# Performance work log

Measured on AMD Instinct MI355X. Metric: run time of the kernel, lower is better.

## Reference

```python
import jax, jax.numpy as jnp
import numpy as np

N, E, IN_DIM, H, C, ED = 100000, 1600000, 128, 8, 16, 16
LN_EPS = 1e-5


def setup_inputs() -> dict:
    key = jax.random.key(0)
    ks = jax.random.split(key, 12)
    s_in = 1.0 / np.sqrt(IN_DIM)
    s_ed = 1.0 / np.sqrt(ED)
    return {
        "edge_index": jax.random.randint(ks[0], (2, E), 0, N, dtype=jnp.int64),
        "point_attr": jax.random.normal(ks[1], (N, IN_DIM), dtype=jnp.float32),
        "edge_attr": jax.random.normal(ks[2], (E, ED), dtype=jnp.float32),
        "W": jax.random.normal(ks[3], (IN_DIM, H * C), dtype=jnp.float32) * s_in,
        "att_src": jax.random.normal(ks[4], (1, H, C), dtype=jnp.float32) * 0.1,
        "att_dst": jax.random.normal(ks[5], (1, H, C), dtype=jnp.float32) * 0.1,
        "W_edge": jax.random.normal(ks[6], (ED, H * C), dtype=jnp.float32) * s_ed,
        "att_edge": jax.random.normal(ks[7], (1, H, C), dtype=jnp.float32) * 0.1,
        "bias": jnp.zeros((H * C,), dtype=jnp.float32),
        "ln_node_g": jnp.ones((H * C,), dtype=jnp.float32),
        "ln_node_b": jnp.zeros((H * C,), dtype=jnp.float32),
        "ln_edge_g": jnp.ones((H,), dtype=jnp.float32),
        "ln_edge_b": jnp.zeros((H,), dtype=jnp.float32),
        "edge_w": jax.random.normal(ks[8], (H, 1), dtype=jnp.float32) / np.sqrt(H),
        "edge_b": jnp.zeros((1,), dtype=jnp.float32),
    }


def _layer_norm(x, g, b):
    mu = jnp.mean(x, axis=-1, keepdims=True)
    var = jnp.mean((x - mu) ** 2, axis=-1, keepdims=True)
    return (x - mu) * jax.lax.rsqrt(var + LN_EPS) * g + b


def reference(edge_index, point_attr, edge_attr, W, att_src, att_dst, W_edge,
              att_edge, bias, ln_node_g, ln_node_b, ln_edge_g, ln_edge_b,
              edge_w, edge_b):
    src, dst = edge_index[0], edge_index[1]
    x = (point_attr @ W).reshape(N, H, C)                 # [N,H,C]
    a_src = jnp.sum(x * att_src, axis=-1)                 # [N,H]
    a_dst = jnp.sum(x * att_dst, axis=-1)                 # [N,H]
    e = (edge_attr @ W_edge).reshape(E, H, C)             # [E,H,C]
    a_edge = jnp.sum(e * att_edge, axis=-1)               # [E,H]
    alpha = jax.nn.leaky_relu(a_src[src] + a_dst[dst] + a_edge, 0.2)
    # segment softmax over destination neighborhoods
    m = jax.ops.segment_max(alpha, dst, num_segments=N)
    m = jnp.where(jnp.isfinite(m), m, 0.0)
    ex = jnp.exp(alpha - m[dst])
    den = jax.ops.segment_sum(ex, dst, num_segments=N)
    alpha_n = ex / (den[dst] + 1e-16)                     # [E,H]
    msg = x[src] * alpha_n[..., None]                     # [E,H,C]
    out = jax.ops.segment_sum(msg, dst, num_segments=N).reshape(N, H * C) + bias
    node_out = jax.nn.leaky_relu(_layer_norm(out, ln_node_g, ln_node_b), 0.01)
    edge_h = _layer_norm(alpha_n, ln_edge_g, ln_edge_b)
    edge_out = jax.nn.relu(edge_h @ edge_w + edge_b)[:, 0]  # [E]
    return node_out, edge_out
```

## Files before the change

kernel.cpp:

```cpp
#include <hip/hip_runtime.h>
#include <hip/hip_bf16.h>

#define NN 100000
#define EE 1600000
#define LN_EPS 1e-5f

__device__ __forceinline__ float bf_lo(unsigned u) {
  union { unsigned i; float f; } c; c.i = u << 16; return c.f;
}
__device__ __forceinline__ float bf_hi(unsigned u) {
  union { unsigned i; float f; } c; c.i = u & 0xffff0000u; return c.f;
}
__device__ __forceinline__ float us_bf(unsigned short u) {
  union { unsigned i; float f; } c; c.i = ((unsigned)u) << 16; return c.f;
}
__device__ __forceinline__ unsigned short f2bf(float f) {
  union { float f; unsigned i; } c; c.f = f;
  unsigned b = c.i + 0x7fffu + ((c.i >> 16) & 1u);
  return (unsigned short)(b >> 16);
}
__device__ __forceinline__ float lrelu02(float v) { return v >= 0.f ? v : 0.2f * v; }

__global__ void k_detect(const void* __restrict__ ei, int* __restrict__ flag) {
  if (threadIdx.x == 0 && blockIdx.x == 0) {
    const unsigned long long* p = (const unsigned long long*)ei;
    int ok = 1;
    for (int i = 0; i < 256; ++i)
      if (p[i] >= (unsigned long long)NN) { ok = 0; break; }
    *flag = ok;
  }
}

__global__ __launch_bounds__(256) void k_convert_hist(const void* __restrict__ ei,
                                                      const int* __restrict__ flag,
                                                      int* __restrict__ idx32,
                                                      int* __restrict__ counts,
                                                      int* __restrict__ rank) {
  int gid = blockIdx.x * 256 + threadIdx.x;
  if (gid >= EE) return;
  int s, d;
  if (*flag) {
    s = (int)((const long long*)ei)[gid];
    d = (int)((const long long*)ei)[EE + gid];
  } else {
    s = ((const int*)ei)[gid];
    d = ((const int*)ei)[EE + gid];
  }
  idx32[gid] = s;
  idx32[EE + gid] = d;
  rank[gid] = atomicAdd(&counts[(unsigned)d * 16], 1);
}

__global__ __launch_bounds__(512) void k_gemm_node(
    const float* __restrict__ P, const float* __restrict__ W,
    const float* __restrict__ attS, const float* __restrict__ attD,
    unsigned* __restrict__ xb, unsigned short* __restrict__ a_srcb,
    unsigned short* __restrict__ a_dstb, int nrows) {
  __shared__ float Rl[32 * 66];
  int t = threadIdx.x;
  int w = __builtin_amdgcn_readfirstlane(t >> 6);
  int l = t & 63;
  int rb = blockIdx.x * 64;
  int cb = w * 16;
  float acc[16];
#pragma unroll
  for (int j = 0; j < 16; ++j) acc[j] = 0.f;

  for (int kc = 0; kc < 4; ++kc) {
    __syncthreads();
    {
      int row = t >> 3;
      int k0 = (t & 7) * 4;
      int grow = rb + row;
      float4 v = make_float4(0.f, 0.f, 0.f, 0.f);
      if (grow < nrows)
        v = *(const float4*)(P + (size_t)grow * 128 + kc * 32 + k0);
      Rl[(k0 + 0) * 66 + row] = v.x;
      Rl[(k0 + 1) * 66 + row] = v.y;
      Rl[(k0 + 2) * 66 + row] = v.z;
      Rl[(k0 + 3) * 66 + row] = v.w;
    }
    __syncthreads();
    const float* Wp = W + (size_t)(kc * 32) * 128 + cb;
#pragma unroll 8
    for (int k = 0; k < 32; ++k) {
      float rv = Rl[k * 66 + l];
#pragma unroll
      for (int j = 0; j < 16; ++j) acc[j] = fmaf(rv, Wp[k * 128 + j], acc[j]);
    }
  }
  int row = rb + l;
  if (row < nrows) {
    float sa = 0.f, sd = 0.f;
#pragma unroll
    for (int j = 0; j < 16; ++j) {
      sa = fmaf(acc[j], attS[cb + j], sa);
      sd = fmaf(acc[j], attD[cb + j], sd);
    }
    a_srcb[(size_t)row * 8 + w] = f2bf(sa);
    a_dstb[(size_t)row * 8 + w] = f2bf(sd);
    unsigned pk[8];
#pragma unroll
    for (int m = 0; m < 8; ++m)
      pk[m] = (unsigned)f2bf(acc[2 * m]) | ((unsigned)f2bf(acc[2 * m + 1]) << 16);
    unsigned* xo = xb + (size_t)row * 64 + cb / 2;
    *(uint4*)(xo) = make_uint4(pk[0], pk[1], pk[2], pk[3]);
    *(uint4*)(xo + 4) = make_uint4(pk[4], pk[5], pk[6], pk[7]);
  }
}

__global__ __launch_bounds__(256) void k_blocksum(const int* __restrict__ counts,
                                                  int* __restrict__ partials, int n) {
  __shared__ int sm[256];
  int t = threadIdx.x;
  int gid = blockIdx.x * 256 + t;
  sm[t] = gid < n ? counts[(unsigned)gid * 16] : 0;
  __syncthreads();
  for (int s = 128; s > 0; s >>= 1) {
    if (t < s) sm[t] += sm[t + s];
    __syncthreads();
  }
  if (t == 0) partials[blockIdx.x] = sm[0];
}

__global__ __launch_bounds__(512) void k_scanpartials(int* __restrict__ partials, int nb) {
  __shared__ int sm[512];
  int t = threadIdx.x;
  int v = t < nb ? partials[t] : 0;
  sm[t] = v;
  __syncthreads();
  for (int off = 1; off < 512; off <<= 1) {
    int u = (t >= off) ? sm[t - off] : 0;
    __syncthreads();
    sm[t] += u;
    __syncthreads();
  }
  if (t < nb) partials[t] = sm[t] - v;
}

__global__ __launch_bounds__(256) void k_scanfinal(const int* __restrict__ counts,
                                                   const int* __restrict__ partials,
                                                   int* __restrict__ offsets, int n) {
  __shared__ int sm[256];
  int t = threadIdx.x;
  int gid = blockIdx.x * 256 + t;
  int v = gid < n ? counts[(unsigned)gid * 16] : 0;
  sm[t] = v;
  __syncthreads();
  for (int off = 1; off < 256; off <<= 1) {
    int u = (t >= off) ? sm[t - off] : 0;
    __syncthreads();
    sm[t] += u;
    __syncthreads();
  }
  int excl = partials[blockIdx.x] + sm[t] - v;
  if (gid < n) offsets[gid] = excl;
  if (gid == n - 1) offsets[n] = excl + v;
}

__global__ __launch_bounds__(256) void k_edgeprep(
    const float* __restrict__ EA, const float* __restrict__ Wedge,
    const float* __restrict__ attE, const int* __restrict__ src,
    const int* __restrict__ dst, const unsigned short* __restrict__ a_srcb,
    const int* __restrict__ offsets, const int* __restrict__ rank,
    unsigned* __restrict__ rec) {
  __shared__ float M[16][8];
  int t = threadIdx.x;
  if (t < 128) {
    int d = t >> 3, h = t & 7;
    float s = 0.f;
#pragma unroll
    for (int c = 0; c < 16; ++c)
      s = fmaf(Wedge[d * 128 + h * 16 + c], attE[h * 16 + c], s);
    M[d][h] = s;
  }
  __syncthreads();
  int stride = gridDim.x * 256;
  for (int e = blockIdx.x * 256 + t; e < EE; e += stride) {
    int sv = src[e], dv = dst[e];
    int rk = rank[e];
    int off = offsets[dv];
    uint4 as4 = *(const uint4*)(a_srcb + (unsigned)sv * 8);
    float ea[16];
    const float4* ea4 = (const float4*)(EA + (size_t)e * 16);
#pragma unroll
    for (int i = 0; i < 4; ++i) {
      float4 v = ea4[i];
      ea[i * 4] = v.x; ea[i * 4 + 1] = v.y; ea[i * 4 + 2] = v.z; ea[i * 4 + 3] = v.w;
    }
    unsigned asu[4] = {as4.x, as4.y, as4.z, as4.w};
    unsigned pk[4];
#pragma unroll
    for (int m = 0; m < 4; ++m) {
      float s0 = 0.f, s1 = 0.f;
#pragma unroll
      for (int d = 0; d < 16; ++d) {
        s0 = fmaf(ea[d], M[d][2 * m], s0);
        s1 = fmaf(ea[d], M[d][2 * m + 1], s1);
      }
      s0 += bf_lo(asu[m]);
      s1 += bf_hi(asu[m]);
      pk[m] = (unsigned)f2bf(s0) | ((unsigned)f2bf(s1) << 16);
    }
    unsigned pos = (unsigned)(off + rk);
    unsigned* rp = rec + (size_t)pos * 8;
    *(uint4*)(rp) = make_uint4(pk[0], pk[1], pk[2], pk[3]);
    *(uint4*)(rp + 4) = make_uint4((unsigned)sv, (unsigned)e, (unsigned)dv, 0u);
  }
}

__global__ __launch_bounds__(512) void k_megaagg(
    const int* __restrict__ offsets, const unsigned* __restrict__ rec,
    const unsigned short* __restrict__ a_dstb, const unsigned* __restrict__ xb,
    const float* __restrict__ bias, const float* __restrict__ g,
    const float* __restrict__ b, const float* __restrict__ eg,
    const float* __restrict__ ebv_, const float* __restrict__ ew,
    const float* __restrict__ ebias, float* __restrict__ node_out,
    float* __restrict__ edge_out) {
  int w = threadIdx.x >> 6, l = threadIdx.x & 63;
  int n = blockIdx.x * 8 + w;
  if (n >= NN) return;
  int s = offsets[n], e = offsets[n + 1];
  int qt = l >> 4, ql = l & 15;
  int h = ql >> 1;
  int hsel = (ql >> 1) & 1;
  unsigned hw = (unsigned)(ql >> 2);
  float ad = us_bf(a_dstb[(unsigned)n * 8 + h]);
  float dn0 = 0.f, dn1 = 0.f, dn2 = 0.f, dn3 = 0.f;
  float acc[8] = {0.f, 0.f, 0.f, 0.f, 0.f, 0.f, 0.f, 0.f};
  int i = s + qt;
  for (; i + 12 < e; i += 16) {
    const unsigned* rA = rec + (unsigned)i * 8u;
    const unsigned* rB = rec + (unsigned)(i + 4) * 8u;
    const unsigned* rC = rec + (unsigned)(i + 8) * 8u;
    const unsigned* rD = rec + (unsigned)(i + 12) * 8u;
    unsigned auA = rA[hw]; unsigned svA = rA[4];
    unsigned auB = rB[hw]; unsigned svB = rB[4];
    unsigned auC = rC[hw]; unsigned svC = rC[4];
    unsigned auD = rD[hw]; unsigned svD = rD[4];
    uint4 xA = *(const uint4*)(xb + svA * 64u + (unsigned)(ql * 4));
    uint4 xB = *(const uint4*)(xb + svB * 64u + (unsigned)(ql * 4));
    uint4 xC = *(const uint4*)(xb + svC * 64u + (unsigned)(ql * 4));
    uint4 xD = *(const uint4*)(xb + svD * 64u + (unsigned)(ql * 4));
    float aA = hsel ? bf_hi(auA) : bf_lo(auA);
    float aB = hsel ? bf_hi(auB) : bf_lo(auB);
    float aC = hsel ? bf_hi(auC) : bf_lo(auC);
    float aD = hsel ? bf_hi(auD) : bf_lo(auD);
    float eA = __expf(lrelu02(aA + ad));
    float eB = __expf(lrelu02(aB + ad));
    float eC = __expf(lrelu02(aC + ad));
    float eD = __expf(lrelu02(aD + ad));
    dn0 += eA; dn1 += eB; dn2 += eC; dn3 += eD;
    acc[0] = fmaf(eA, bf_lo(xA.x), acc[0]); acc[1] = fmaf(eA, bf_hi(xA.x), acc[1]);
    acc[2] = fmaf(eA, bf_lo(xA.y), acc[2]); acc[3] = fmaf(eA, bf_hi(xA.y), acc[3]);
    acc[4] = fmaf(eA, bf_lo(xA.z), acc[4]); acc[5] = fmaf(eA, bf_hi(xA.z), acc[5]);
    acc[6] = fmaf(eA, bf_lo(xA.w), acc[6]); acc[7] = fmaf(eA, bf_hi(xA.w), acc[7]);
    acc[0] = fmaf(eB, bf_lo(xB.x), acc[0]); acc[1] = fmaf(eB, bf_hi(xB.x), acc[1]);
    acc[2] = fmaf(eB, bf_lo(xB.y), acc[2]); acc[3] = fmaf(eB, bf_hi(xB.y), acc[3]);
    acc[4] = fmaf(eB, bf_lo(xB.z), acc[4]); acc[5] = fmaf(eB, bf_hi(xB.z), acc[5]);
    acc[6] = fmaf(eB, bf_lo(xB.w), acc[6]); acc[7] = fmaf(eB, bf_hi(xB.w), acc[7]);
    acc[0] = fmaf(eC, bf_lo(xC.x), acc[0]); acc[1] = fmaf(eC, bf_hi(xC.x), acc[1]);
    acc[2] = fmaf(eC, bf_lo(xC.y), acc[2]); acc[3] = fmaf(eC, bf_hi(xC.y), acc[3]);
    acc[4] = fmaf(eC, bf_lo(xC.z), acc[4]); acc[5] = fmaf(eC, bf_hi(xC.z), acc[5]);
    acc[6] = fmaf(eC, bf_lo(xC.w), acc[6]); acc[7] = fmaf(eC, bf_hi(xC.w), acc[7]);
    acc[0] = fmaf(eD, bf_lo(xD.x), acc[0]); acc[1] = fmaf(eD, bf_hi(xD.x), acc[1]);
    acc[2] = fmaf(eD, bf_lo(xD.y), acc[2]); acc[3] = fmaf(eD, bf_hi(xD.y), acc[3]);
    acc[4] = fmaf(eD, bf_lo(xD.z), acc[4]); acc[5] = fmaf(eD, bf_hi(xD.z), acc[5]);
    acc[6] = fmaf(eD, bf_lo(xD.w), acc[6]); acc[7] = fmaf(eD, bf_hi(xD.w), acc[7]);
  }
  for (; i < e; i += 4) {
    const unsigned* rA = rec + (unsigned)i * 8u;
    unsigned auA = rA[hw]; unsigned svA = rA[4];
    uint4 xA = *(const uint4*)(xb + svA * 64u + (unsigned)(ql * 4));
    float aA = hsel ? bf_hi(auA) : bf_lo(auA);
    float eA = __expf(lrelu02(aA + ad));
    dn0 += eA;
    acc[0] = fmaf(eA, bf_lo(xA.x), acc[0]); acc[1] = fmaf(eA, bf_hi(xA.x), acc[1]);
    acc[2] = fmaf(eA, bf_lo(xA.y), acc[2]); acc[3] = fmaf(eA, bf_hi(xA.y), acc[3]);
    acc[4] = fmaf(eA, bf_lo(xA.z), acc[4]); acc[5] = fmaf(eA, bf_hi(xA.z), acc[5]);
    acc[6] = fmaf(eA, bf_lo(xA.w), acc[6]); acc[7] = fmaf(eA, bf_hi(xA.w), acc[7]);
  }
  float den = (dn0 + dn1) + (dn2 + dn3);
  den += __shfl_xor(den, 16);
  den += __shfl_xor(den, 32);
#pragma unroll
  for (int j = 0; j < 8; ++j) {
    acc[j] += __shfl_xor(acc[j], 16);
    acc[j] += __shfl_xor(acc[j], 32);
  }
  float inv = 1.f / (den + 1e-16f);
  int c0 = ql * 8;
  float4 bv0 = *(const float4*)(bias + c0);
  float4 bv1 = *(const float4*)(bias + c0 + 4);
  acc[0] = acc[0] * inv + bv0.x;
  acc[1] = acc[1] * inv + bv0.y;
  acc[2] = acc[2] * inv + bv0.z;
  acc[3] = acc[3] * inv + bv0.w;
  acc[4] = acc[4] * inv + bv1.x;
  acc[5] = acc[5] * inv + bv1.y;
  acc[6] = acc[6] * inv + bv1.z;
  acc[7] = acc[7] * inv + bv1.w;
  float sum = ((acc[0] + acc[1]) + (acc[2] + acc[3])) +
              ((acc[4] + acc[5]) + (acc[6] + acc[7]));
#pragma unroll
  for (int off = 1; off < 64; off <<= 1) sum += __shfl_xor(sum, off);
  float mu = sum * (1.f / 512.f);
  float d[8], ss = 0.f;
#pragma unroll
  for (int j = 0; j < 8; ++j) { d[j] = acc[j] - mu; ss += d[j] * d[j]; }
#pragma unroll
  for (int off = 1; off < 64; off <<= 1) ss += __shfl_xor(ss, off);
  float r = rsqrtf(ss * (1.f / 512.f) + LN_EPS);
  if (qt == 0) {
    float4 gv0 = *(const float4*)(g + c0);
    float4 gv1 = *(const float4*)(g + c0 + 4);
    float4 bb0 = *(const float4*)(b + c0);
    float4 bb1 = *(const float4*)(b + c0 + 4);
    float y[8];
    y[0] = d[0] * r * gv0.x + bb0.x;
    y[1] = d[1] * r * gv0.y + bb0.y;
    y[2] = d[2] * r * gv0.z + bb0.z;
    y[3] = d[3] * r * gv0.w + bb0.w;
    y[4] = d[4] * r * gv1.x + bb1.x;
    y[5] = d[5] * r * gv1.y + bb1.y;
    y[6] = d[6] * r * gv1.z + bb1.z;
    y[7] = d[7] * r * gv1.w + bb1.w;
#pragma unroll
    for (int j = 0; j < 8; ++j) y[j] = y[j] >= 0.f ? y[j] : 0.01f * y[j];
    float* no = node_out + (size_t)n * 128 + c0;
    *(float4*)(no) = make_float4(y[0], y[1], y[2], y[3]);
    *(float4*)(no + 4) = make_float4(y[4], y[5], y[6], y[7]);
  }
  float invs[8];
#pragma unroll
  for (int hh = 0; hh < 8; ++hh) invs[hh] = __shfl(inv, hh * 2);
  uint4 adu4 = *(const uint4*)(a_dstb + (unsigned)n * 8);
  unsigned adu[4] = {adu4.x, adu4.y, adu4.z, adu4.w};
  float gw[8];
  float bsum = ebias[0];
#pragma unroll
  for (int hh = 0; hh < 8; ++hh) {
    float ewv = ew[hh];
    gw[hh] = eg[hh] * ewv;
    bsum += ebv_[hh] * ewv;
  }
  for (int i2 = s + l; i2 < e; i2 += 64) {
    const unsigned* rp = rec + (unsigned)i2 * 8u;
    uint4 as4 = *(const uint4*)(rp);
    unsigned eidx = rp[5];
    unsigned asu[4] = {as4.x, as4.y, as4.z, as4.w};
    float p[8];
#pragma unroll
    for (int m = 0; m < 4; ++m) {
      float a0 = lrelu02(bf_lo(asu[m]) + bf_lo(adu[m]));
      float a1 = lrelu02(bf_hi(asu[m]) + bf_hi(adu[m]));
      p[2 * m] = __expf(a0) * invs[2 * m];
      p[2 * m + 1] = __expf(a1) * invs[2 * m + 1];
    }
    float pm = 0.f;
#pragma unroll
    for (int hh = 0; hh < 8; ++hh) pm += p[hh];
    pm *= 0.125f;
    float var = 0.f, dot = 0.f;
#pragma unroll
    for (int hh = 0; hh < 8; ++hh) {
      float dd = p[hh] - pm;
      var += dd * dd;
      dot += dd * gw[hh];
    }
    var *= 0.125f;
    float rr = rsqrtf(var + LN_EPS);
    float o = dot * rr + bsum;
    edge_out[eidx] = fmaxf(o, 0.f);
  }
}

extern "C" void kernel_launch(void* const* d_in, const int* in_sizes, int n_in,
                              void* d_out, int out_size, void* d_ws, size_t ws_size,
                              hipStream_t stream) {
  const void* edge_index = d_in[0];
  const float* point_attr = (const float*)d_in[1];
  const float* edge_attr = (const float*)d_in[2];
  const float* W = (const float*)d_in[3];
  const float* att_src = (const float*)d_in[4];
  const float* att_dst = (const float*)d_in[5];
  const float* W_edge = (const float*)d_in[6];
  const float* att_edge = (const float*)d_in[7];
  const float* bias = (const float*)d_in[8];
  const float* ln_node_g = (const float*)d_in[9];
  const float* ln_node_b = (const float*)d_in[10];
  const float* ln_edge_g = (const float*)d_in[11];
  const float* ln_edge_b = (const float*)d_in[12];
  const float* edge_w = (const float*)d_in[13];
  const float* edge_b = (const float*)d_in[14];

  char* wsb = (char*)d_ws;
  size_t o = 0;
  auto take = [&](size_t bytes) -> void* {
    void* p = wsb + o;
    o += (bytes + 255) & ~(size_t)255;
    return p;
  };
  int* flag = (int*)take(4);
  int* idx32 = (int*)take((size_t)2 * EE * 4);
  unsigned* xb = (unsigned*)take((size_t)NN * 128 * 2);
  unsigned short* a_srcb = (unsigned short*)take((size_t)NN * 8 * 2);
  unsigned short* a_dstb = (unsigned short*)take((size_t)NN * 8 * 2);
  int* counts = (int*)take((size_t)NN * 16 * 4);
  int* offsets = (int*)take((size_t)(NN + 1) * 4);
  int* rank = (int*)take((size_t)EE * 4);
  int* partials = (int*)take(512 * 4);
  unsigned* rec = (unsigned*)take((size_t)EE * 32);

  const int* srcp = idx32;
  const int* dstp = idx32 + EE;
  float* node_out = (float*)d_out;
  float* edge_out = node_out + (size_t)NN * 128;

  int nb_scan = (NN + 255) / 256;

  hipMemsetAsync(counts, 0, (size_t)NN * 16 * 4, stream);

  k_detect<<<1, 64, 0, stream>>>(edge_index, flag);
  k_convert_hist<<<(EE + 255) / 256, 256, 0, stream>>>(edge_index, flag, idx32,
                                                       counts, rank);
  k_gemm_node<<<(NN + 63) / 64, 512, 0, stream>>>(point_attr, W, att_src, att_dst,
                                                  xb, a_srcb, a_dstb, NN);
  k_blocksum<<<nb_scan, 256, 0, stream>>>(counts, partials, NN);
  k_scanpartials<<<1, 512, 0, stream>>>(partials, nb_scan);
  k_scanfinal<<<nb_scan, 256, 0, stream>>>(counts, partials, offsets, NN);
  k_edgeprep<<<2048, 256, 0, stream>>>(edge_attr, W_edge, att_edge, srcp, dstp,
                                       a_srcb, offsets, rank, rec);
  k_megaagg<<<(NN + 7) / 8, 512, 0, stream>>>(offsets, rec, a_dstb, xb, bias,
                                              ln_node_g, ln_node_b, ln_edge_g,
                                              ln_edge_b, edge_w, edge_b,
                                              node_out, edge_out);
}
```

Before: 333.9 us.

## Precompute exp attention weights in edge prep and grid-stride the histogram

Edge prep now gathers a_dst per edge and stores exp(leaky_relu(logit)) in bf16 in each record, instead of the raw source logit. The aggregation kernel reads these weights directly, which removes the exp computation from both its gather loop and its edge-output loop. The histogram kernel becomes a grid-stride loop over 2048 blocks. The cost is one extra random a_dst gather per edge, and storing exp values without max-subtraction in bf16 can overflow or lose precision for large logits (the code before also skipped the max).

```diff
diff --git a/kernel.cpp b/kernel.cpp
--- a/kernel.cpp
+++ b/kernel.cpp
@@ -36,19 +36,21 @@
                                                       int* __restrict__ idx32,
                                                       int* __restrict__ counts,
                                                       int* __restrict__ rank) {
-  int gid = blockIdx.x * 256 + threadIdx.x;
-  if (gid >= EE) return;
-  int s, d;
-  if (*flag) {
-    s = (int)((const long long*)ei)[gid];
-    d = (int)((const long long*)ei)[EE + gid];
-  } else {
-    s = ((const int*)ei)[gid];
-    d = ((const int*)ei)[EE + gid];
-  }
-  idx32[gid] = s;
-  idx32[EE + gid] = d;
-  rank[gid] = atomicAdd(&counts[(unsigned)d * 16], 1);
+  int stride = gridDim.x * 256;
+  int i64 = *flag;
+  for (int gid = blockIdx.x * 256 + threadIdx.x; gid < EE; gid += stride) {
+    int s, d;
+    if (i64) {
+      s = (int)((const long long*)ei)[gid];
+      d = (int)((const long long*)ei)[EE + gid];
+    } else {
+      s = ((const int*)ei)[gid];
+      d = ((const int*)ei)[EE + gid];
+    }
+    idx32[gid] = s;
+    idx32[EE + gid] = d;
+    rank[gid] = atomicAdd(&counts[(unsigned)d * 16], 1);
+  }
 }
 
 __global__ __launch_bounds__(512) void k_gemm_node(
@@ -162,8 +164,8 @@
     const float* __restrict__ EA, const float* __restrict__ Wedge,
     const float* __restrict__ attE, const int* __restrict__ src,
     const int* __restrict__ dst, const unsigned short* __restrict__ a_srcb,
-    const int* __restrict__ offsets, const int* __restrict__ rank,
-    unsigned* __restrict__ rec) {
+    const unsigned short* __restrict__ a_dstb, const int* __restrict__ offsets,
+    const int* __restrict__ rank, unsigned* __restrict__ rec) {
   __shared__ float M[16][8];
   int t = threadIdx.x;
   if (t < 128) {
@@ -181,6 +183,7 @@
     int rk = rank[e];
     int off = offsets[dv];
     uint4 as4 = *(const uint4*)(a_srcb + (unsigned)sv * 8);
+    uint4 ad4 = *(const uint4*)(a_dstb + (unsigned)dv * 8);
     float ea[16];
     const float4* ea4 = (const float4*)(EA + (size_t)e * 16);
 #pragma unroll
@@ -189,6 +192,7 @@
       ea[i * 4] = v.x; ea[i * 4 + 1] = v.y; ea[i * 4 + 2] = v.z; ea[i * 4 + 3] = v.w;
     }
     unsigned asu[4] = {as4.x, as4.y, as4.z, as4.w};
+    unsigned adu[4] = {ad4.x, ad4.y, ad4.z, ad4.w};
     unsigned pk[4];
 #pragma unroll
     for (int m = 0; m < 4; ++m) {
@@ -198,9 +202,11 @@
         s0 = fmaf(ea[d], M[d][2 * m], s0);
         s1 = fmaf(ea[d], M[d][2 * m + 1], s1);
       }
-      s0 += bf_lo(asu[m]);
-      s1 += bf_hi(asu[m]);
-      pk[m] = (unsigned)f2bf(s0) | ((unsigned)f2bf(s1) << 16);
+      s0 += bf_lo(asu[m]) + bf_lo(adu[m]);
+      s1 += bf_hi(asu[m]) + bf_hi(adu[m]);
+      float w0 = __expf(lrelu02(s0));
+      float w1 = __expf(lrelu02(s1));
+      pk[m] = (unsigned)f2bf(w0) | ((unsigned)f2bf(w1) << 16);
     }
     unsigned pos = (unsigned)(off + rk);
     unsigned* rp = rec + (size_t)pos * 8;
@@ -211,74 +217,60 @@
 
 __global__ __launch_bounds__(512) void k_megaagg(
     const int* __restrict__ offsets, const unsigned* __restrict__ rec,
-    const unsigned short* __restrict__ a_dstb, const unsigned* __restrict__ xb,
-    const float* __restrict__ bias, const float* __restrict__ g,
-    const float* __restrict__ b, const float* __restrict__ eg,
-    const float* __restrict__ ebv_, const float* __restrict__ ew,
-    const float* __restrict__ ebias, float* __restrict__ node_out,
-    float* __restrict__ edge_out) {
+    const unsigned* __restrict__ xb, const float* __restrict__ bias,
+    const float* __restrict__ g, const float* __restrict__ b,
+    const float* __restrict__ eg, const float* __restrict__ ebv_,
+    const float* __restrict__ ew, const float* __restrict__ ebias,
+    float* __restrict__ node_out, float* __restrict__ edge_out) {
   int w = threadIdx.x >> 6, l = threadIdx.x & 63;
   int n = blockIdx.x * 8 + w;
   if (n >= NN) return;
   int s = offsets[n], e = offsets[n + 1];
   int qt = l >> 4, ql = l & 15;
   int h = ql >> 1;
-  int hsel = (ql >> 1) & 1;
-  unsigned hw = (unsigned)(ql >> 2);
-  float ad = us_bf(a_dstb[(unsigned)n * 8 + h]);
   float dn0 = 0.f, dn1 = 0.f, dn2 = 0.f, dn3 = 0.f;
   float acc[8] = {0.f, 0.f, 0.f, 0.f, 0.f, 0.f, 0.f, 0.f};
   int i = s + qt;
   for (; i + 12 < e; i += 16) {
-    const unsigned* rA = rec + (unsigned)i * 8u;
-    const unsigned* rB = rec + (unsigned)(i + 4) * 8u;
-    const unsigned* rC = rec + (unsigned)(i + 8) * 8u;
-    const unsigned* rD = rec + (unsigned)(i + 12) * 8u;
-    unsigned auA = rA[hw]; unsigned svA = rA[4];
-    unsigned auB = rB[hw]; unsigned svB = rB[4];
-    unsigned auC = rC[hw]; unsigned svC = rC[4];
-    unsigned auD = rD[hw]; unsigned svD = rD[4];
+    const unsigned short* rA = (const unsigned short*)(rec + (unsigned)i * 8u);
+    const unsigned short* rB = (const unsigned short*)(rec + (unsigned)(i + 4) * 8u);
+    const unsigned short* rC = (const unsigned short*)(rec + (unsigned)(i + 8) * 8u);
+    const unsigned short* rD = (const unsigned short*)(rec + (unsigned)(i + 12) * 8u);
+    float wA = us_bf(rA[h]); unsigned svA = ((const unsigned*)rA)[4];
+    float wB = us_bf(rB[h]); unsigned svB = ((const unsigned*)rB)[4];
+    float wC = us_bf(rC[h]); unsigned svC = ((const unsigned*)rC)[4];
+    float wD = us_bf(rD[h]); unsigned svD = ((const unsigned*)rD)[4];
     uint4 xA = *(const uint4*)(xb + svA * 64u + (unsigned)(ql * 4));
     uint4 xB = *(const uint4*)(xb + svB * 64u + (unsigned)(ql * 4));
     uint4 xC = *(const uint4*)(xb + svC * 64u + (unsigned)(ql * 4));
     uint4 xD = *(const uint4*)(xb + svD * 64u + (unsigned)(ql * 4));
-    float aA = hsel ? bf_hi(auA) : bf_lo(auA);
-    float aB = hsel ? bf_hi(auB) : bf_lo(auB);
-    float aC = hsel ? bf_hi(auC) : bf_lo(auC);
-    float aD = hsel ? bf_hi(auD) : bf_lo(auD);
-    float eA = __expf(lrelu02(aA + ad));
-    float eB = __expf(lrelu02(aB + ad));
-    float eC = __expf(lrelu02(aC + ad));
-    float eD = __expf(lrelu02(aD + ad));
-    dn0 += eA; dn1 += eB; dn2 += eC; dn3 += eD;
-    acc[0] = fmaf(eA, bf_lo(xA.x), acc[0]); acc[1] = fmaf(eA, bf_hi(xA.x), acc[1]);
-    acc[2] = fmaf(eA, bf_lo(xA.y), acc[2]); acc[3] = fmaf(eA, bf_hi(xA.y), acc[3]);
-    acc[4] = fmaf(eA, bf_lo(xA.z), acc[4]); acc[5] = fmaf(eA, bf_hi(xA.z), acc[5]);
-    acc[6] = fmaf(eA, bf_lo(xA.w), acc[6]); acc[7] = fmaf(eA, bf_hi(xA.w), acc[7]);
-    acc[0] = fmaf(eB, bf_lo(xB.x), acc[0]); acc[1] = fmaf(eB, bf_hi(xB.x), acc[1]);
-    acc[2] = fmaf(eB, bf_lo(xB.y), acc[2]); acc[3] = fmaf(eB, bf_hi(xB.y), acc[3]);
-    acc[4] = fmaf(eB, bf_lo(xB.z), acc[4]); acc[5] = fmaf(eB, bf_hi(xB.z), acc[5]);
-    acc[6] = fmaf(eB, bf_lo(xB.w), acc[6]); acc[7] = fmaf(eB, bf_hi(xB.w), acc[7]);
-    acc[0] = fmaf(eC, bf_lo(xC.x), acc[0]); acc[1] = fmaf(eC, bf_hi(xC.x), acc[1]);
-    acc[2] = fmaf(eC, bf_lo(xC.y), acc[2]); acc[3] = fmaf(eC, bf_hi(xC.y), acc[3]);
-    acc[4] = fmaf(eC, bf_lo(xC.z), acc[4]); acc[5] = fmaf(eC, bf_hi(xC.z), acc[5]);
-    acc[6] = fmaf(eC, bf_lo(xC.w), acc[6]); acc[7] = fmaf(eC, bf_hi(xC.w), acc[7]);
-    acc[0] = fmaf(eD, bf_lo(xD.x), acc[0]); acc[1] = fmaf(eD, bf_hi(xD.x), acc[1]);
-    acc[2] = fmaf(eD, bf_lo(xD.y), acc[2]); acc[3] = fmaf(eD, bf_hi(xD.y), acc[3]);
-    acc[4] = fmaf(eD, bf_lo(xD.z), acc[4]); acc[5] = fmaf(eD, bf_hi(xD.z), acc[5]);
-    acc[6] = fmaf(eD, bf_lo(xD.w), acc[6]); acc[7] = fmaf(eD, bf_hi(xD.w), acc[7]);
+    dn0 += wA; dn1 += wB; dn2 += wC; dn3 += wD;
+    acc[0] = fmaf(wA, bf_lo(xA.x), acc[0]); acc[1] = fmaf(wA, bf_hi(xA.x), acc[1]);
+    acc[2] = fmaf(wA, bf_lo(xA.y), acc[2]); acc[3] = fmaf(wA, bf_hi(xA.y), acc[3]);
+    acc[4] = fmaf(wA, bf_lo(xA.z), acc[4]); acc[5] = fmaf(wA, bf_hi(xA.z), acc[5]);
+    acc[6] = fmaf(wA, bf_lo(xA.w), acc[6]); acc[7] = fmaf(wA, bf_hi(xA.w), acc[7]);
+    acc[0] = fmaf(wB, bf_lo(xB.x), acc[0]); acc[1] = fmaf(wB, bf_hi(xB.x), acc[1]);
+    acc[2] = fmaf(wB, bf_lo(xB.y), acc[2]); acc[3] = fmaf(wB, bf_hi(xB.y), acc[3]);
+    acc[4] = fmaf(wB, bf_lo(xB.z), acc[4]); acc[5] = fmaf(wB, bf_hi(xB.z), acc[5]);
+    acc[6] = fmaf(wB, bf_lo(xB.w), acc[6]); acc[7] = fmaf(wB, bf_hi(xB.w), acc[7]);
+    acc[0] = fmaf(wC, bf_lo(xC.x), acc[0]); acc[1] = fmaf(wC, bf_hi(xC.x), acc[1]);
+    acc[2] = fmaf(wC, bf_lo(xC.y), acc[2]); acc[3] = fmaf(wC, bf_hi(xC.y), acc[3]);
+    acc[4] = fmaf(wC, bf_lo(xC.z), acc[4]); acc[5] = fmaf(wC, bf_hi(xC.z), acc[5]);
+    acc[6] = fmaf(wC, bf_lo(xC.w), acc[6]); acc[7] = fmaf(wC, bf_hi(xC.w), acc[7]);
+    acc[0] = fmaf(wD, bf_lo(xD.x), acc[0]); acc[1] = fmaf(wD, bf_hi(xD.x), acc[1]);
+    acc[2] = fmaf(wD, bf_lo(xD.y), acc[2]); acc[3] = fmaf(wD, bf_hi(xD.y), acc[3]);
+    acc[4] = fmaf(wD, bf_lo(xD.z), acc[4]); acc[5] = fmaf(wD, bf_hi(xD.z), acc[5]);
+    acc[6] = fmaf(wD, bf_lo(xD.w), acc[6]); acc[7] = fmaf(wD, bf_hi(xD.w), acc[7]);
   }
   for (; i < e; i += 4) {
-    const unsigned* rA = rec + (unsigned)i * 8u;
-    unsigned auA = rA[hw]; unsigned svA = rA[4];
+    const unsigned short* rA = (const unsigned short*)(rec + (unsigned)i * 8u);
+    float wA = us_bf(rA[h]); unsigned svA = ((const unsigned*)rA)[4];
     uint4 xA = *(const uint4*)(xb + svA * 64u + (unsigned)(ql * 4));
-    float aA = hsel ? bf_hi(auA) : bf_lo(auA);
-    float eA = __expf(lrelu02(aA + ad));
-    dn0 += eA;
-    acc[0] = fmaf(eA, bf_lo(xA.x), acc[0]); acc[1] = fmaf(eA, bf_hi(xA.x), acc[1]);
-    acc[2] = fmaf(eA, bf_lo(xA.y), acc[2]); acc[3] = fmaf(eA, bf_hi(xA.y), acc[3]);
-    acc[4] = fmaf(eA, bf_lo(xA.z), acc[4]); acc[5] = fmaf(eA, bf_hi(xA.z), acc[5]);
-    acc[6] = fmaf(eA, bf_lo(xA.w), acc[6]); acc[7] = fmaf(eA, bf_hi(xA.w), acc[7]);
+    dn0 += wA;
+    acc[0] = fmaf(wA, bf_lo(xA.x), acc[0]); acc[1] = fmaf(wA, bf_hi(xA.x), acc[1]);
+    acc[2] = fmaf(wA, bf_lo(xA.y), acc[2]); acc[3] = fmaf(wA, bf_hi(xA.y), acc[3]);
+    acc[4] = fmaf(wA, bf_lo(xA.z), acc[4]); acc[5] = fmaf(wA, bf_hi(xA.z), acc[5]);
+    acc[6] = fmaf(wA, bf_lo(xA.w), acc[6]); acc[7] = fmaf(wA, bf_hi(xA.w), acc[7]);
   }
   float den = (dn0 + dn1) + (dn2 + dn3);
   den += __shfl_xor(den, 16);
@@ -334,8 +326,6 @@
   float invs[8];
 #pragma unroll
   for (int hh = 0; hh < 8; ++hh) invs[hh] = __shfl(inv, hh * 2);
-  uint4 adu4 = *(const uint4*)(a_dstb + (unsigned)n * 8);
-  unsigned adu[4] = {adu4.x, adu4.y, adu4.z, adu4.w};
   float gw[8];
   float bsum = ebias[0];
 #pragma unroll
@@ -346,16 +336,14 @@
   }
   for (int i2 = s + l; i2 < e; i2 += 64) {
     const unsigned* rp = rec + (unsigned)i2 * 8u;
-    uint4 as4 = *(const uint4*)(rp);
+    uint4 w4 = *(const uint4*)(rp);
     unsigned eidx = rp[5];
-    unsigned asu[4] = {as4.x, as4.y, as4.z, as4.w};
+    unsigned wu[4] = {w4.x, w4.y, w4.z, w4.w};
     float p[8];
 #pragma unroll
     for (int m = 0; m < 4; ++m) {
-      float a0 = lrelu02(bf_lo(asu[m]) + bf_lo(adu[m]));
-      float a1 = lrelu02(bf_hi(asu[m]) + bf_hi(adu[m]));
-      p[2 * m] = __expf(a0) * invs[2 * m];
-      p[2 * m + 1] = __expf(a1) * invs[2 * m + 1];
+      p[2 * m] = bf_lo(wu[m]) * invs[2 * m];
+      p[2 * m + 1] = bf_hi(wu[m]) * invs[2 * m + 1];
     }
     float pm = 0.f;
 #pragma unroll
@@ -422,16 +410,15 @@
   hipMemsetAsync(counts, 0, (size_t)NN * 16 * 4, stream);
 
   k_detect<<<1, 64, 0, stream>>>(edge_index, flag);
-  k_convert_hist<<<(EE + 255) / 256, 256, 0, stream>>>(edge_index, flag, idx32,
-                                                       counts, rank);
+  k_convert_hist<<<2048, 256, 0, stream>>>(edge_index, flag, idx32, counts, rank);
   k_gemm_node<<<(NN + 63) / 64, 512, 0, stream>>>(point_attr, W, att_src, att_dst,
                                                   xb, a_srcb, a_dstb, NN);
   k_blocksum<<<nb_scan, 256, 0, stream>>>(counts, partials, NN);
   k_scanpartials<<<1, 512, 0, stream>>>(partials, nb_scan);
   k_scanfinal<<<nb_scan, 256, 0, stream>>>(counts, partials, offsets, NN);
   k_edgeprep<<<2048, 256, 0, stream>>>(edge_attr, W_edge, att_edge, srcp, dstp,
-                                       a_srcb, offsets, rank, rec);
-  k_megaagg<<<(NN + 7) / 8, 512, 0, stream>>>(offsets, rec, a_dstb, xb, bias,
+                                       a_srcb, a_dstb, offsets, rank, rec);
+  k_megaagg<<<(NN + 7) / 8, 512, 0, stream>>>(offsets, rec, xb, bias,
                                               ln_node_g, ln_node_b, ln_edge_g,
                                               ln_edge_b, edge_w, edge_b,
                                               node_out, edge_out);
```

Measured after the change: 358.2 us. +7.3%, slower.
